# Optimization experiments

Hardware: AMD Instinct MI355X
Metric: run time of the kernel (lower is better)

## Reference

```python
import jax, jax.numpy as jnp
import numpy as np

EMBED_DIM = 64  # scale factor dim (matches head dim)


def setup_inputs() -> dict:
    key0 = jax.random.key(0)
    kq, kk, kv = jax.random.split(key0, 3)
    shape = (2, 16, 2048, 64)  # [B, H, S, D]
    return {
        "query": jax.random.normal(kq, shape, dtype=jnp.float32),
        "key": jax.random.normal(kk, shape, dtype=jnp.float32),
        "value": jax.random.normal(kv, shape, dtype=jnp.float32),
    }


def reference(query, key, value):
    # qk = Q K^T / sqrt(embed_dim); softmax over last dim; @ V
    inv_scale = jnp.sqrt(jnp.asarray(EMBED_DIM, dtype=query.dtype))
    scores = jnp.einsum("bhqd,bhkd->bhqk", query, key) / inv_scale
    probs = jax.nn.softmax(scores, axis=-1)
    # dropout_p=0.0 -> identity (eval semantics)
    return jnp.einsum("bhqk,bhkd->bhqd", probs, value)
```

## Files before the change

### kernel.cpp

```cpp
#include <hip/hip_runtime.h>
#include <hip/hip_bf16.h>

#define S_LEN 2048
#define DDIM  64
#define NT    (S_LEN / 64)
#define SCALE  0.125f
#define SCALE2 0.18033688f
#define NELEM  4194304
#define NQROW  65536
#define WC_LGKM0 0xc07f

#if __has_builtin(__builtin_amdgcn_permlane32_swap) && __has_builtin(__builtin_amdgcn_permlane16_swap)
#define HAVE_PLSWAP 1
#else
#define HAVE_PLSWAP 0
#endif

typedef __attribute__((ext_vector_type(8))) short short8;
typedef __attribute__((ext_vector_type(4))) float floatx4;

__device__ __forceinline__ short f2bf(float f) {
    union { float f; unsigned u; } v; v.f = f;
    return (short)((v.u + 0x7fffu + ((v.u >> 16) & 1u)) >> 16);
}

__device__ __forceinline__ unsigned pk2bf(float a, float b) {
#if __has_builtin(__builtin_amdgcn_cvt_pk_bf16_f32)
    auto r = __builtin_amdgcn_cvt_pk_bf16_f32(a, b);
    union { decltype(r) v; unsigned u; } c; c.v = v.v, c.v = r; return c.u;
#else
    union { float f; unsigned u; } x, y; x.f = a; y.f = b;
    unsigned lo = (x.u + 0x7fffu + ((x.u >> 16) & 1u)) >> 16;
    unsigned hi = (y.u + 0x7fffu + ((y.u >> 16) & 1u)) & 0xffff0000u;
    return lo | hi;
#endif
}

__device__ __forceinline__ float fexp2(float x) {
#if __has_builtin(__builtin_amdgcn_exp2f)
    return __builtin_amdgcn_exp2f(x);
#else
    return exp2f(x);
#endif
}

#if HAVE_PLSWAP
__device__ __forceinline__ void plswap32(unsigned &a, unsigned &b) {
    auto r = __builtin_amdgcn_permlane32_swap((int)a, (int)b, false, false);
    a = (unsigned)r[0]; b = (unsigned)r[1];
}
__device__ __forceinline__ void plswap16(unsigned &a, unsigned &b) {
    auto r = __builtin_amdgcn_permlane16_swap((int)a, (int)b, false, false);
    a = (unsigned)r[0]; b = (unsigned)r[1];
}
#endif

__global__ __launch_bounds__(256) void prep_kv(const float* __restrict__ K,
                                               const float* __restrict__ V,
                                               short* __restrict__ Kb,
                                               short* __restrict__ Vt) {
    const int bh = blockIdx.x & 31;
    const int st = blockIdx.x >> 5;
    const int t  = threadIdx.x;
    const size_t tile_off = (size_t)bh * (S_LEN * DDIM) + (size_t)st * (64 * DDIM);

    {
        const float* src = K + tile_off + t * 16;
        short* dst = Kb + tile_off + t * 16;
        #pragma unroll
        for (int h = 0; h < 2; ++h) {
            float4 a = *(const float4*)(src + h * 8);
            float4 b = *(const float4*)(src + h * 8 + 4);
            uint4 o;
            o.x = pk2bf(a.x, a.y); o.y = pk2bf(a.z, a.w);
            o.z = pk2bf(b.x, b.y); o.w = pk2bf(b.z, b.w);
            *(uint4*)(dst + h * 8) = o;
        }
    }

    {
        const int s4 = (t & 15) * 4;
        const int d4 = (t >> 4) * 4;
        const float* src = V + tile_off;
        float4 v0 = *(const float4*)(src + (size_t)(s4 + 0) * 64 + d4);
        float4 v1 = *(const float4*)(src + (size_t)(s4 + 1) * 64 + d4);
        float4 v2 = *(const float4*)(src + (size_t)(s4 + 2) * 64 + d4);
        float4 v3 = *(const float4*)(src + (size_t)(s4 + 3) * 64 + d4);
        const float* r0 = (const float*)&v0;
        const float* r1 = (const float*)&v1;
        const float* r2 = (const float*)&v2;
        const float* r3 = (const float*)&v3;
        short* dstb = Vt + (size_t)bh * (DDIM * S_LEN) + (size_t)st * 64 + s4;
        #pragma unroll
        for (int dd = 0; dd < 4; ++dd) {
            uint2 o;
            o.x = pk2bf(r0[dd], r1[dd]);
            o.y = pk2bf(r2[dd], r3[dd]);
            *(uint2*)(dstb + (size_t)(d4 + dd) * S_LEN) = o;
        }
    }
}

template <int NSPLIT>
__global__ __launch_bounds__(256) void attn_sm(
    const float* __restrict__ Q, const short* __restrict__ Kb,
    const short* __restrict__ Vt, float* __restrict__ O,
    float* __restrict__ numer, float* __restrict__ denom)
{
    __shared__ short Ks[64 * 64];
    __shared__ short Vs[64 * 64];
#if !HAVE_PLSWAP
    __shared__ short Pl[4][32 * 64];
#endif

    constexpr int NIT = NT / NSPLIT;

    const int tid  = threadIdx.x;
    const int wave = tid >> 6;
    const int lane = tid & 63;
    const int l16  = lane & 15;
    const int quad = lane >> 4;
    const int x7   = l16 & 7;

    const int bh = blockIdx.x & 31;
    const int rest = blockIdx.x >> 5;
    const int qt = rest & 15;
    const int ks = rest >> 4;
    const size_t base = (size_t)bh * (S_LEN * DDIM);

    const int ci0 = tid,        r0 = ci0 >> 3, c0 = (ci0 & 7) ^ (r0 & 7);
    const int ci1 = 256 + tid,  r1 = ci1 >> 3, c1 = (ci1 & 7) ^ (r1 & 7);
    const size_t koff = (size_t)ks * NIT * (64 * 64);
    const size_t voff = (size_t)ks * NIT * 64;
    const short* pK0 = Kb + base + koff + r0 * 64 + c0 * 8;
    const short* pK1 = Kb + base + koff + r1 * 64 + c1 * 8;
    const short* pV0 = Vt + base + voff + (size_t)r0 * S_LEN + c0 * 8;
    const short* pV1 = Vt + base + voff + (size_t)r1 * S_LEN + c1 * 8;

    short8 rk0 = *(const short8*)pK0;
    short8 rk1 = *(const short8*)pK1;
    short8 rv0 = *(const short8*)pV0;
    short8 rv1 = *(const short8*)pV1;

    short8 qf[2][2];
    #pragma unroll
    for (int nq = 0; nq < 2; ++nq) {
        const float* qp = Q + base + (size_t)(qt * 128 + wave * 32 + nq * 16 + l16) * 64 + quad * 8;
        #pragma unroll
        for (int kt = 0; kt < 2; ++kt) {
            float4 a = *(const float4*)(qp + kt * 32);
            float4 b = *(const float4*)(qp + kt * 32 + 4);
            union { unsigned u[4]; short8 s; } qc;
            qc.u[0] = pk2bf(a.x * SCALE2, a.y * SCALE2);
            qc.u[1] = pk2bf(a.z * SCALE2, a.w * SCALE2);
            qc.u[2] = pk2bf(b.x * SCALE2, b.y * SCALE2);
            qc.u[3] = pk2bf(b.z * SCALE2, b.w * SCALE2);
            qf[nq][kt] = qc.s;
        }
    }

    floatx4 oacc[2][4];
    float rs[2];
    #pragma unroll
    for (int mt = 0; mt < 2; ++mt) {
        #pragma unroll
        for (int dt = 0; dt < 4; ++dt) oacc[mt][dt] = (floatx4){0.f,0.f,0.f,0.f};
        rs[mt] = 0.f;
    }

#if !HAVE_PLSWAP
    short* Pw = &Pl[wave][0];
#endif

    for (int kb = 0; kb < NIT; ++kb) {
        if (kb) __builtin_amdgcn_s_barrier();

        *(short8*)&Ks[ci0 * 8] = rk0;
        *(short8*)&Ks[ci1 * 8] = rk1;
        *(short8*)&Vs[ci0 * 8] = rv0;
        *(short8*)&Vs[ci1 * 8] = rv1;

        if (kb + 1 < NIT) {
            const int ok = (kb + 1) * (64 * 64), ov = (kb + 1) * 64;
            rk0 = *(const short8*)(pK0 + ok);
            rk1 = *(const short8*)(pK1 + ok);
            rv0 = *(const short8*)(pV0 + ov);
            rv1 = *(const short8*)(pV1 + ov);
        }

        __builtin_amdgcn_s_waitcnt(WC_LGKM0);
        __builtin_amdgcn_s_barrier();

        floatx4 sc[2][4];
        #pragma unroll
        for (int mk = 0; mk < 4; ++mk) {
            floatx4 a0 = (floatx4){0.f,0.f,0.f,0.f};
            floatx4 a1 = (floatx4){0.f,0.f,0.f,0.f};
            #pragma unroll
            for (int kt = 0; kt < 2; ++kt) {
                const int csw = (kt * 4 + quad) ^ x7;
                short8 kf = *(const short8*)&Ks[(mk * 16 + l16) * 64 + csw * 8];
                a0 = __builtin_amdgcn_mfma_f32_16x16x32_bf16(kf, qf[0][kt], a0, 0, 0, 0);
                a1 = __builtin_amdgcn_mfma_f32_16x16x32_bf16(kf, qf[1][kt], a1, 0, 0, 0);
            }
            sc[0][mk] = a0; sc[1][mk] = a1;
        }

#if HAVE_PLSWAP
        unsigned pa[2][4], pb[2][4];
        #pragma unroll
        for (int nq = 0; nq < 2; ++nq) {
            #pragma unroll
            for (int mk = 0; mk < 4; ++mk) {
                float p0 = fexp2(sc[nq][mk][0]);
                float p1 = fexp2(sc[nq][mk][1]);
                float p2 = fexp2(sc[nq][mk][2]);
                float p3 = fexp2(sc[nq][mk][3]);
                rs[nq] += (p0 + p1) + (p2 + p3);
                pa[nq][mk] = pk2bf(p0, p1);
                pb[nq][mk] = pk2bf(p2, p3);
            }
        }

        #pragma unroll
        for (int kt = 0; kt < 2; ++kt) {
            short8 pf[2];
            #pragma unroll
            for (int nq = 0; nq < 2; ++nq) {
                unsigned a0 = pa[nq][2 * kt], a1 = pa[nq][2 * kt + 1];
                unsigned b0 = pb[nq][2 * kt], b1 = pb[nq][2 * kt + 1];
                plswap32(a0, a1); plswap16(a0, a1);
                plswap32(b0, b1); plswap16(b0, b1);
                union { unsigned u[4]; short8 s; } c;
                c.u[0] = a0; c.u[1] = b0; c.u[2] = a1; c.u[3] = b1;
                pf[nq] = c.s;
            }
            const int csw = (kt * 4 + quad) ^ x7;
            #pragma unroll
            for (int dt = 0; dt < 4; ++dt) {
                short8 vf = *(const short8*)&Vs[(dt * 16 + l16) * 64 + csw * 8];
                oacc[0][dt] = __builtin_amdgcn_mfma_f32_16x16x32_bf16(pf[0], vf, oacc[0][dt], 0, 0, 0);
                oacc[1][dt] = __builtin_amdgcn_mfma_f32_16x16x32_bf16(pf[1], vf, oacc[1][dt], 0, 0, 0);
            }
        }
#else
        #pragma unroll
        for (int nq = 0; nq < 2; ++nq) {
            const int prow = (nq * 16 + l16) * 64;
            #pragma unroll
            for (int mk = 0; mk < 4; ++mk) {
                float p0 = fexp2(sc[nq][mk][0]);
                float p1 = fexp2(sc[nq][mk][1]);
                float p2 = fexp2(sc[nq][mk][2]);
                float p3 = fexp2(sc[nq][mk][3]);
                rs[nq] += (p0 + p1) + (p2 + p3);
                uint2 pv; pv.x = pk2bf(p0, p1); pv.y = pk2bf(p2, p3);
                const int c8 = (mk * 4 + quad) ^ (2 * x7);
                *(uint2*)&Pw[prow + c8 * 4] = pv;
            }
        }
        #pragma unroll
        for (int kt = 0; kt < 2; ++kt) {
            const int csw = (kt * 4 + quad) ^ x7;
            short8 pf0 = *(const short8*)&Pw[(l16)      * 64 + csw * 8];
            short8 pf1 = *(const short8*)&Pw[(16 + l16) * 64 + csw * 8];
            #pragma unroll
            for (int dt = 0; dt < 4; ++dt) {
                short8 vf = *(const short8*)&Vs[(dt * 16 + l16) * 64 + csw * 8];
                oacc[0][dt] = __builtin_amdgcn_mfma_f32_16x16x32_bf16(pf0, vf, oacc[0][dt], 0, 0, 0);
                oacc[1][dt] = __builtin_amdgcn_mfma_f32_16x16x32_bf16(pf1, vf, oacc[1][dt], 0, 0, 0);
            }
        }
#endif
    }

    float inv[2];
    #pragma unroll
    for (int nq = 0; nq < 2; ++nq) {
        float s = rs[nq];
        s += __shfl_xor(s, 16, 64);
        s += __shfl_xor(s, 32, 64);
        if (NSPLIT == 2) {
            if (quad == 0)
                denom[(size_t)ks * NQROW + bh * S_LEN + qt * 128 + wave * 32 + nq * 16 + l16] = s;
        }
        inv[nq] = 1.0f / s;
    }

    #pragma unroll
    for (int mt = 0; mt < 2; ++mt) {
        #pragma unroll
        for (int r = 0; r < 4; ++r) {
            const int row = qt * 128 + wave * 32 + mt * 16 + quad * 4 + r;
            if (NSPLIT == 1) {
                const float d_r = __shfl(inv[mt], quad * 4 + r, 64);
                float* op = O + base + (size_t)row * 64 + l16;
                #pragma unroll
                for (int dt = 0; dt < 4; ++dt)
                    op[dt * 16] = oacc[mt][dt][r] * d_r;
            } else {
                float* np = numer + (size_t)ks * NELEM + base + (size_t)row * 64 + l16;
                #pragma unroll
                for (int dt = 0; dt < 4; ++dt)
                    np[dt * 16] = oacc[mt][dt][r];
            }
        }
    }
}

__global__ __launch_bounds__(256) void combine2(const float* __restrict__ numer,
                                                const float* __restrict__ denom,
                                                float* __restrict__ O) {
    const size_t i = ((size_t)blockIdx.x * 256 + threadIdx.x) * 4;
    const size_t q = i >> 6;
    const float inv = 1.0f / (denom[q] + denom[NQROW + q]);
    float4 n0 = *(const float4*)(numer + i);
    float4 n1 = *(const float4*)(numer + NELEM + i);
    float4 o;
    o.x = (n0.x + n1.x) * inv;
    o.y = (n0.y + n1.y) * inv;
    o.z = (n0.z + n1.z) * inv;
    o.w = (n0.w + n1.w) * inv;
    *(float4*)(O + i) = o;
}

#define BQ    64
#define BKEY  64
#define KPAD  72

__global__ __launch_bounds__(256) void attn_kernel(
    const float* __restrict__ Q, const float* __restrict__ K,
    const float* __restrict__ V, float* __restrict__ O)
{
    __shared__ short Ksh[BKEY * KPAD];
    __shared__ short Vtt[DDIM * KPAD];
    __shared__ short Pls[4][16 * KPAD];

    const int tid  = threadIdx.x;
    const int wave = tid >> 6;
    const int lane = tid & 63;
    const int l16  = lane & 15;
    const int quad = lane >> 4;

    const int bh = blockIdx.x & 31;
    const int qt = blockIdx.x >> 5;
    const size_t base = (size_t)bh * S_LEN * DDIM;

    const int qrow = qt * BQ + wave * 16 + l16;
    short8 qf[2];
    {
        const float* qp = Q + base + (size_t)qrow * DDIM + quad * 8;
        #pragma unroll
        for (int kt = 0; kt < 2; ++kt) {
            float4 a = *(const float4*)(qp + kt * 32);
            float4 b = *(const float4*)(qp + kt * 32 + 4);
            short* d = (short*)&qf[kt];
            d[0]=f2bf(a.x*SCALE); d[1]=f2bf(a.y*SCALE); d[2]=f2bf(a.z*SCALE); d[3]=f2bf(a.w*SCALE);
            d[4]=f2bf(b.x*SCALE); d[5]=f2bf(b.y*SCALE); d[6]=f2bf(b.z*SCALE); d[7]=f2bf(b.w*SCALE);
        }
    }

    float m_i[4], l_i[4];
    floatx4 oacc[4];
    #pragma unroll
    for (int r = 0; r < 4; ++r) { m_i[r] = -3.0e38f; l_i[r] = 0.f; }
    #pragma unroll
    for (int dt = 0; dt < 4; ++dt) oacc[dt] = (floatx4){0.f, 0.f, 0.f, 0.f};

    const int skey = tid >> 2;
    const int scol = (tid & 3) * 4;

    for (int kb = 0; kb < S_LEN / BKEY; ++kb) {
        const float* Kg = K + base + (size_t)kb * BKEY * DDIM + (size_t)skey * DDIM;
        const float* Vg = V + base + (size_t)kb * BKEY * DDIM + (size_t)skey * DDIM;
        #pragma unroll
        for (int i = 0; i < 4; ++i) {
            const int c = scol + i * 16;
            float4 kv = *(const float4*)(Kg + c);
            short* kd = &Ksh[skey * KPAD + c];
            kd[0]=f2bf(kv.x); kd[1]=f2bf(kv.y); kd[2]=f2bf(kv.z); kd[3]=f2bf(kv.w);
            float4 vv = *(const float4*)(Vg + c);
            Vtt[(c+0)*KPAD + skey] = f2bf(vv.x);
            Vtt[(c+1)*KPAD + skey] = f2bf(vv.y);
            Vtt[(c+2)*KPAD + skey] = f2bf(vv.z);
            Vtt[(c+3)*KPAD + skey] = f2bf(vv.w);
        }
        __syncthreads();

        floatx4 sc[4];
        #pragma unroll
        for (int nt = 0; nt < 4; ++nt) {
            floatx4 acc = (floatx4){0.f, 0.f, 0.f, 0.f};
            #pragma unroll
            for (int kt = 0; kt < 2; ++kt) {
                short8 kf = *(const short8*)&Ksh[(nt*16 + l16) * KPAD + kt*32 + quad*8];
                acc = __builtin_amdgcn_mfma_f32_16x16x32_bf16(qf[kt], kf, acc, 0, 0, 0);
            }
            sc[nt] = acc;
        }

        short* Pw = &Pls[wave][0];
        #pragma unroll
        for (int r = 0; r < 4; ++r) {
            float mx = fmaxf(fmaxf(sc[0][r], sc[1][r]), fmaxf(sc[2][r], sc[3][r]));
            #pragma unroll
            for (int off = 1; off < 16; off <<= 1)
                mx = fmaxf(mx, __shfl_xor(mx, off, 64));
            const float mnew  = fmaxf(m_i[r], mx);
            const float alpha = __expf(m_i[r] - mnew);
            m_i[r] = mnew;
            float rsum = 0.f;
            #pragma unroll
            for (int nt = 0; nt < 4; ++nt) {
                float p = __expf(sc[nt][r] - mnew);
                rsum += p;
                Pw[(quad*4 + r) * KPAD + nt*16 + l16] = f2bf(p);
            }
            #pragma unroll
            for (int off = 1; off < 16; off <<= 1)
                rsum += __shfl_xor(rsum, off, 64);
            l_i[r] = l_i[r] * alpha + rsum;
            oacc[0][r] *= alpha; oacc[1][r] *= alpha;
            oacc[2][r] *= alpha; oacc[3][r] *= alpha;
        }

        #pragma unroll
        for (int kt = 0; kt < 2; ++kt) {
            short8 pf = *(const short8*)&Pw[l16 * KPAD + kt*32 + quad*8];
            #pragma unroll
            for (int dt = 0; dt < 4; ++dt) {
                short8 vf = *(const short8*)&Vtt[(dt*16 + l16) * KPAD + kt*32 + quad*8];
                oacc[dt] = __builtin_amdgcn_mfma_f32_16x16x32_bf16(pf, vf, oacc[dt], 0, 0, 0);
            }
        }
        __syncthreads();
    }

    #pragma unroll
    for (int r = 0; r < 4; ++r) {
        const float inv = 1.0f / l_i[r];
        const int row = qt * BQ + wave * 16 + quad * 4 + r;
        float* op = O + base + (size_t)row * DDIM + l16;
        #pragma unroll
        for (int dt = 0; dt < 4; ++dt)
            op[dt * 16] = oacc[dt][r] * inv;
    }
}

extern "C" void kernel_launch(void* const* d_in, const int* in_sizes, int n_in,
                              void* d_out, int out_size, void* d_ws, size_t ws_size,
                              hipStream_t stream) {
    const float* Q = (const float*)d_in[0];
    const float* K = (const float*)d_in[1];
    const float* V = (const float*)d_in[2];
    float* O = (float*)d_out;

    const size_t prep_bytes = (size_t)NELEM * 2 * 2;
    const size_t split_bytes = prep_bytes + (size_t)2 * NELEM * 4
                             + (size_t)2 * NQROW * 4;

    if (ws_size >= split_bytes) {
        short* Kb  = (short*)d_ws;
        short* Vtp = (short*)d_ws + NELEM;
        float* num = (float*)((char*)d_ws + prep_bytes);
        float* den = num + (size_t)2 * NELEM;
        prep_kv<<<dim3(1024), dim3(256), 0, stream>>>(K, V, Kb, Vtp);
        attn_sm<2><<<dim3(1024), dim3(256), 0, stream>>>(Q, Kb, Vtp, nullptr, num, den);
        combine2<<<dim3(NELEM / 1024), dim3(256), 0, stream>>>(num, den, O);
    } else if (ws_size >= prep_bytes) {
        short* Kb  = (short*)d_ws;
        short* Vtp = (short*)d_ws + NELEM;
        prep_kv<<<dim3(1024), dim3(256), 0, stream>>>(K, V, Kb, Vtp);
        attn_sm<1><<<dim3(512), dim3(256), 0, stream>>>(Q, Kb, Vtp, O, nullptr, nullptr);
    } else {
        attn_kernel<<<dim3(1024), dim3(256), 0, stream>>>(Q, K, V, O);
    }
}
```

Baseline: 150.7 us.

## Fuse split-K combine into attention kernel via last-arriver atomic counter

```diff
diff --git a/kernel.cpp b/kernel.cpp
--- a/kernel.cpp
+++ b/kernel.cpp
@@ -25,15 +25,10 @@
 }
 
 __device__ __forceinline__ unsigned pk2bf(float a, float b) {
-#if __has_builtin(__builtin_amdgcn_cvt_pk_bf16_f32)
-    auto r = __builtin_amdgcn_cvt_pk_bf16_f32(a, b);
-    union { decltype(r) v; unsigned u; } c; c.v = v.v, c.v = r; return c.u;
-#else
     union { float f; unsigned u; } x, y; x.f = a; y.f = b;
     unsigned lo = (x.u + 0x7fffu + ((x.u >> 16) & 1u)) >> 16;
     unsigned hi = (y.u + 0x7fffu + ((y.u >> 16) & 1u)) & 0xffff0000u;
     return lo | hi;
-#endif
 }
 
 __device__ __forceinline__ float fexp2(float x) {
@@ -58,11 +53,17 @@
 __global__ __launch_bounds__(256) void prep_kv(const float* __restrict__ K,
                                                const float* __restrict__ V,
                                                short* __restrict__ Kb,
-                                               short* __restrict__ Vt) {
+                                               short* __restrict__ Vt,
+                                               unsigned* __restrict__ cnt) {
     const int bh = blockIdx.x & 31;
     const int st = blockIdx.x >> 5;
     const int t  = threadIdx.x;
     const size_t tile_off = (size_t)bh * (S_LEN * DDIM) + (size_t)st * (64 * DDIM);
+
+    if (cnt && blockIdx.x == 0) {
+        cnt[t] = 0u;
+        cnt[t + 256] = 0u;
+    }
 
     {
         const float* src = K + tile_off + t * 16;
@@ -105,10 +106,12 @@
 __global__ __launch_bounds__(256) void attn_sm(
     const float* __restrict__ Q, const short* __restrict__ Kb,
     const short* __restrict__ Vt, float* __restrict__ O,
-    float* __restrict__ numer, float* __restrict__ denom)
+    float* __restrict__ numer, float* __restrict__ denom,
+    unsigned* __restrict__ cnt)
 {
     __shared__ short Ks[64 * 64];
     __shared__ short Vs[64 * 64];
+    __shared__ unsigned sflag;
 #if !HAVE_PLSWAP
     __shared__ short Pl[4][32 * 64];
 #endif
@@ -274,35 +277,74 @@
 #endif
     }
 
-    float inv[2];
+    float sred[2];
     #pragma unroll
     for (int nq = 0; nq < 2; ++nq) {
         float s = rs[nq];
         s += __shfl_xor(s, 16, 64);
         s += __shfl_xor(s, 32, 64);
-        if (NSPLIT == 2) {
-            if (quad == 0)
-                denom[(size_t)ks * NQROW + bh * S_LEN + qt * 128 + wave * 32 + nq * 16 + l16] = s;
-        }
-        inv[nq] = 1.0f / s;
-    }
-
-    #pragma unroll
-    for (int mt = 0; mt < 2; ++mt) {
-        #pragma unroll
-        for (int r = 0; r < 4; ++r) {
-            const int row = qt * 128 + wave * 32 + mt * 16 + quad * 4 + r;
-            if (NSPLIT == 1) {
-                const float d_r = __shfl(inv[mt], quad * 4 + r, 64);
+        sred[nq] = s;
+    }
+
+    if (NSPLIT == 1) {
+        #pragma unroll
+        for (int mt = 0; mt < 2; ++mt) {
+            const float invm = 1.0f / sred[mt];
+            #pragma unroll
+            for (int r = 0; r < 4; ++r) {
+                const int row = qt * 128 + wave * 32 + mt * 16 + quad * 4 + r;
+                const float d_r = __shfl(invm, quad * 4 + r, 64);
                 float* op = O + base + (size_t)row * 64 + l16;
                 #pragma unroll
                 for (int dt = 0; dt < 4; ++dt)
                     op[dt * 16] = oacc[mt][dt][r] * d_r;
-            } else {
+            }
+        }
+    } else {
+        if (quad == 0) {
+            #pragma unroll
+            for (int nq = 0; nq < 2; ++nq)
+                denom[(size_t)ks * NQROW + bh * S_LEN + qt * 128 + wave * 32 + nq * 16 + l16] = sred[nq];
+        }
+        #pragma unroll
+        for (int mt = 0; mt < 2; ++mt) {
+            #pragma unroll
+            for (int r = 0; r < 4; ++r) {
+                const int row = qt * 128 + wave * 32 + mt * 16 + quad * 4 + r;
                 float* np = numer + (size_t)ks * NELEM + base + (size_t)row * 64 + l16;
                 #pragma unroll
                 for (int dt = 0; dt < 4; ++dt)
                     np[dt * 16] = oacc[mt][dt][r];
+            }
+        }
+
+        __threadfence();
+        __syncthreads();
+        if (tid == 0) sflag = atomicAdd(&cnt[(bh << 4) + qt], 1u);
+        __syncthreads();
+        if (sflag == 0) return;
+        __threadfence();
+
+        const int kso = 1 - ks;
+        const float* onum = numer + (size_t)kso * NELEM + base;
+        const float* oden = denom + (size_t)kso * NQROW + bh * S_LEN + qt * 128 + wave * 32;
+
+        float invt[2];
+        #pragma unroll
+        for (int nq = 0; nq < 2; ++nq)
+            invt[nq] = 1.0f / (sred[nq] + oden[nq * 16 + l16]);
+
+        #pragma unroll
+        for (int mt = 0; mt < 2; ++mt) {
+            #pragma unroll
+            for (int r = 0; r < 4; ++r) {
+                const int row = qt * 128 + wave * 32 + mt * 16 + quad * 4 + r;
+                const float it = __shfl(invt[mt], quad * 4 + r, 64);
+                const float* np = onum + (size_t)row * 64 + l16;
+                float* op = O + base + (size_t)row * 64 + l16;
+                #pragma unroll
+                for (int dt = 0; dt < 4; ++dt)
+                    op[dt * 16] = (oacc[mt][dt][r] + np[dt * 16]) * it;
             }
         }
     }
@@ -458,20 +500,29 @@
     const size_t prep_bytes = (size_t)NELEM * 2 * 2;
     const size_t split_bytes = prep_bytes + (size_t)2 * NELEM * 4
                              + (size_t)2 * NQROW * 4;
-
-    if (ws_size >= split_bytes) {
+    const size_t fused_bytes = split_bytes + 2048;
+
+    if (ws_size >= fused_bytes) {
         short* Kb  = (short*)d_ws;
         short* Vtp = (short*)d_ws + NELEM;
         float* num = (float*)((char*)d_ws + prep_bytes);
         float* den = num + (size_t)2 * NELEM;
-        prep_kv<<<dim3(1024), dim3(256), 0, stream>>>(K, V, Kb, Vtp);
-        attn_sm<2><<<dim3(1024), dim3(256), 0, stream>>>(Q, Kb, Vtp, nullptr, num, den);
+        unsigned* cnt = (unsigned*)((char*)d_ws + split_bytes);
+        prep_kv<<<dim3(1024), dim3(256), 0, stream>>>(K, V, Kb, Vtp, cnt);
+        attn_sm<2><<<dim3(1024), dim3(256), 0, stream>>>(Q, Kb, Vtp, O, num, den, cnt);
+    } else if (ws_size >= split_bytes) {
+        short* Kb  = (short*)d_ws;
+        short* Vtp = (short*)d_ws + NELEM;
+        float* num = (float*)((char*)d_ws + prep_bytes);
+        float* den = num + (size_t)2 * NELEM;
+        prep_kv<<<dim3(1024), dim3(256), 0, stream>>>(K, V, Kb, Vtp, nullptr);
+        attn_sm<2><<<dim3(1024), dim3(256), 0, stream>>>(Q, Kb, Vtp, nullptr, num, den, nullptr);
         combine2<<<dim3(NELEM / 1024), dim3(256), 0, stream>>>(num, den, O);
     } else if (ws_size >= prep_bytes) {
         short* Kb  = (short*)d_ws;
         short* Vtp = (short*)d_ws + NELEM;
-        prep_kv<<<dim3(1024), dim3(256), 0, stream>>>(K, V, Kb, Vtp);
-        attn_sm<1><<<dim3(512), dim3(256), 0, stream>>>(Q, Kb, Vtp, O, nullptr, nullptr);
+        prep_kv<<<dim3(1024), dim3(256), 0, stream>>>(K, V, Kb, Vtp, nullptr);
+        attn_sm<1><<<dim3(512), dim3(256), 0, stream>>>(Q, Kb, Vtp, O, nullptr, nullptr, nullptr);
     } else {
         attn_kernel<<<dim3(1024), dim3(256), 0, stream>>>(Q, K, V, O);
     }
```

After: 307.2 us. 104% more time.

## Fuse split-K attention halves into one 512-thread block with LDS combine

Applied to the files above, without the earlier changes.

```diff
diff --git a/kernel.cpp b/kernel.cpp
--- a/kernel.cpp
+++ b/kernel.cpp
@@ -25,15 +25,10 @@
 }
 
 __device__ __forceinline__ unsigned pk2bf(float a, float b) {
-#if __has_builtin(__builtin_amdgcn_cvt_pk_bf16_f32)
-    auto r = __builtin_amdgcn_cvt_pk_bf16_f32(a, b);
-    union { decltype(r) v; unsigned u; } c; c.v = v.v, c.v = r; return c.u;
-#else
     union { float f; unsigned u; } x, y; x.f = a; y.f = b;
     unsigned lo = (x.u + 0x7fffu + ((x.u >> 16) & 1u)) >> 16;
     unsigned hi = (y.u + 0x7fffu + ((y.u >> 16) & 1u)) & 0xffff0000u;
     return lo | hi;
-#endif
 }
 
 __device__ __forceinline__ float fexp2(float x) {
@@ -101,35 +96,36 @@
     }
 }
 
-template <int NSPLIT>
-__global__ __launch_bounds__(256) void attn_sm(
+__global__ __launch_bounds__(512) void attn_sm8(
     const float* __restrict__ Q, const short* __restrict__ Kb,
-    const short* __restrict__ Vt, float* __restrict__ O,
-    float* __restrict__ numer, float* __restrict__ denom)
+    const short* __restrict__ Vt, float* __restrict__ O)
 {
-    __shared__ short Ks[64 * 64];
-    __shared__ short Vs[64 * 64];
+    __shared__ short Ks[2][64 * 64];
+    __shared__ short Vs[2][64 * 64];
+    __shared__ float Dl[128];
 #if !HAVE_PLSWAP
-    __shared__ short Pl[4][32 * 64];
-#endif
-
-    constexpr int NIT = NT / NSPLIT;
+    __shared__ short Pl[8][32 * 64];
+#endif
+
+    constexpr int NIT = NT / 2;
 
     const int tid  = threadIdx.x;
     const int wave = tid >> 6;
+    const int grp  = wave >> 2;
+    const int w4   = wave & 3;
     const int lane = tid & 63;
     const int l16  = lane & 15;
     const int quad = lane >> 4;
     const int x7   = l16 & 7;
 
     const int bh = blockIdx.x & 31;
-    const int rest = blockIdx.x >> 5;
-    const int qt = rest & 15;
-    const int ks = rest >> 4;
+    const int qt = blockIdx.x >> 5;
+    const int ks = grp;
     const size_t base = (size_t)bh * (S_LEN * DDIM);
 
-    const int ci0 = tid,        r0 = ci0 >> 3, c0 = (ci0 & 7) ^ (r0 & 7);
-    const int ci1 = 256 + tid,  r1 = ci1 >> 3, c1 = (ci1 & 7) ^ (r1 & 7);
+    const int g   = tid & 255;
+    const int ci0 = g,        r0 = ci0 >> 3, c0 = (ci0 & 7) ^ (r0 & 7);
+    const int ci1 = 256 + g,  r1 = ci1 >> 3, c1 = (ci1 & 7) ^ (r1 & 7);
     const size_t koff = (size_t)ks * NIT * (64 * 64);
     const size_t voff = (size_t)ks * NIT * 64;
     const short* pK0 = Kb + base + koff + r0 * 64 + c0 * 8;
@@ -145,7 +141,7 @@
     short8 qf[2][2];
     #pragma unroll
     for (int nq = 0; nq < 2; ++nq) {
-        const float* qp = Q + base + (size_t)(qt * 128 + wave * 32 + nq * 16 + l16) * 64 + quad * 8;
+        const float* qp = Q + base + (size_t)(qt * 128 + w4 * 32 + nq * 16 + l16) * 64 + quad * 8;
         #pragma unroll
         for (int kt = 0; kt < 2; ++kt) {
             float4 a = *(const float4*)(qp + kt * 32);
@@ -168,6 +164,8 @@
         rs[mt] = 0.f;
     }
 
+    short* Ksg = &Ks[grp][0];
+    short* Vsg = &Vs[grp][0];
 #if !HAVE_PLSWAP
     short* Pw = &Pl[wave][0];
 #endif
@@ -175,10 +173,10 @@
     for (int kb = 0; kb < NIT; ++kb) {
         if (kb) __builtin_amdgcn_s_barrier();
 
-        *(short8*)&Ks[ci0 * 8] = rk0;
-        *(short8*)&Ks[ci1 * 8] = rk1;
-        *(short8*)&Vs[ci0 * 8] = rv0;
-        *(short8*)&Vs[ci1 * 8] = rv1;
+        *(short8*)&Ksg[ci0 * 8] = rk0;
+        *(short8*)&Ksg[ci1 * 8] = rk1;
+        *(short8*)&Vsg[ci0 * 8] = rv0;
+        *(short8*)&Vsg[ci1 * 8] = rv1;
 
         if (kb + 1 < NIT) {
             const int ok = (kb + 1) * (64 * 64), ov = (kb + 1) * 64;
@@ -199,7 +197,7 @@
             #pragma unroll
             for (int kt = 0; kt < 2; ++kt) {
                 const int csw = (kt * 4 + quad) ^ x7;
-                short8 kf = *(const short8*)&Ks[(mk * 16 + l16) * 64 + csw * 8];
+                short8 kf = *(const short8*)&Ksg[(mk * 16 + l16) * 64 + csw * 8];
                 a0 = __builtin_amdgcn_mfma_f32_16x16x32_bf16(kf, qf[0][kt], a0, 0, 0, 0);
                 a1 = __builtin_amdgcn_mfma_f32_16x16x32_bf16(kf, qf[1][kt], a1, 0, 0, 0);
             }
@@ -238,7 +236,7 @@
             const int csw = (kt * 4 + quad) ^ x7;
             #pragma unroll
             for (int dt = 0; dt < 4; ++dt) {
-                short8 vf = *(const short8*)&Vs[(dt * 16 + l16) * 64 + csw * 8];
+                short8 vf = *(const short8*)&Vsg[(dt * 16 + l16) * 64 + csw * 8];
                 oacc[0][dt] = __builtin_amdgcn_mfma_f32_16x16x32_bf16(pf[0], vf, oacc[0][dt], 0, 0, 0);
                 oacc[1][dt] = __builtin_amdgcn_mfma_f32_16x16x32_bf16(pf[1], vf, oacc[1][dt], 0, 0, 0);
             }
@@ -266,7 +264,7 @@
             short8 pf1 = *(const short8*)&Pw[(16 + l16) * 64 + csw * 8];
             #pragma unroll
             for (int dt = 0; dt < 4; ++dt) {
-                short8 vf = *(const short8*)&Vs[(dt * 16 + l16) * 64 + csw * 8];
+                short8 vf = *(const short8*)&Vsg[(dt * 16 + l16) * 64 + csw * 8];
                 oacc[0][dt] = __builtin_amdgcn_mfma_f32_16x16x32_bf16(pf0, vf, oacc[0][dt], 0, 0, 0);
                 oacc[1][dt] = __builtin_amdgcn_mfma_f32_16x16x32_bf16(pf1, vf, oacc[1][dt], 0, 0, 0);
             }
@@ -274,54 +272,51 @@
 #endif
     }
 
-    float inv[2];
+    float sred[2];
     #pragma unroll
     for (int nq = 0; nq < 2; ++nq) {
         float s = rs[nq];
         s += __shfl_xor(s, 16, 64);
         s += __shfl_xor(s, 32, 64);
-        if (NSPLIT == 2) {
-            if (quad == 0)
-                denom[(size_t)ks * NQROW + bh * S_LEN + qt * 128 + wave * 32 + nq * 16 + l16] = s;
-        }
-        inv[nq] = 1.0f / s;
-    }
-
+        sred[nq] = s;
+    }
+
+    if (grp == 1 && quad == 0) {
+        Dl[w4 * 32 + l16]      = sred[0];
+        Dl[w4 * 32 + 16 + l16] = sred[1];
+    }
+    __syncthreads();
+
+    float invt[2];
+    if (grp == 0) {
+        invt[0] = 1.0f / (sred[0] + Dl[w4 * 32 + l16]);
+        invt[1] = 1.0f / (sred[1] + Dl[w4 * 32 + 16 + l16]);
+    }
+
+    float* Nb = (float*)&Ks[0][0];
     #pragma unroll
     for (int mt = 0; mt < 2; ++mt) {
-        #pragma unroll
-        for (int r = 0; r < 4; ++r) {
-            const int row = qt * 128 + wave * 32 + mt * 16 + quad * 4 + r;
-            if (NSPLIT == 1) {
-                const float d_r = __shfl(inv[mt], quad * 4 + r, 64);
+        if (grp == 1) {
+            #pragma unroll
+            for (int dt = 0; dt < 4; ++dt)
+                #pragma unroll
+                for (int r = 0; r < 4; ++r)
+                    Nb[(dt * 4 + r) * 256 + w4 * 64 + lane] = oacc[mt][dt][r];
+        }
+        __syncthreads();
+        if (grp == 0) {
+            #pragma unroll
+            for (int r = 0; r < 4; ++r) {
+                const int row = qt * 128 + w4 * 32 + mt * 16 + quad * 4 + r;
+                const float it = __shfl(invt[mt], quad * 4 + r, 64);
                 float* op = O + base + (size_t)row * 64 + l16;
                 #pragma unroll
                 for (int dt = 0; dt < 4; ++dt)
-                    op[dt * 16] = oacc[mt][dt][r] * d_r;
-            } else {
-                float* np = numer + (size_t)ks * NELEM + base + (size_t)row * 64 + l16;
-                #pragma unroll
-                for (int dt = 0; dt < 4; ++dt)
-                    np[dt * 16] = oacc[mt][dt][r];
-            }
-        }
-    }
-}
-
-__global__ __launch_bounds__(256) void combine2(const float* __restrict__ numer,
-                                                const float* __restrict__ denom,
-                                                float* __restrict__ O) {
-    const size_t i = ((size_t)blockIdx.x * 256 + threadIdx.x) * 4;
-    const size_t q = i >> 6;
-    const float inv = 1.0f / (denom[q] + denom[NQROW + q]);
-    float4 n0 = *(const float4*)(numer + i);
-    float4 n1 = *(const float4*)(numer + NELEM + i);
-    float4 o;
-    o.x = (n0.x + n1.x) * inv;
-    o.y = (n0.y + n1.y) * inv;
-    o.z = (n0.z + n1.z) * inv;
-    o.w = (n0.w + n1.w) * inv;
-    *(float4*)(O + i) = o;
+                    op[dt * 16] = (oacc[mt][dt][r] + Nb[(dt * 4 + r) * 256 + w4 * 64 + lane]) * it;
+            }
+        }
+        __syncthreads();
+    }
 }
 
 #define BQ    64
@@ -456,22 +451,12 @@
     float* O = (float*)d_out;
 
     const size_t prep_bytes = (size_t)NELEM * 2 * 2;
-    const size_t split_bytes = prep_bytes + (size_t)2 * NELEM * 4
-                             + (size_t)2 * NQROW * 4;
-
-    if (ws_size >= split_bytes) {
-        short* Kb  = (short*)d_ws;
-        short* Vtp = (short*)d_ws + NELEM;
-        float* num = (float*)((char*)d_ws + prep_bytes);
-        float* den = num + (size_t)2 * NELEM;
-        prep_kv<<<dim3(1024), dim3(256), 0, stream>>>(K, V, Kb, Vtp);
-        attn_sm<2><<<dim3(1024), dim3(256), 0, stream>>>(Q, Kb, Vtp, nullptr, num, den);
-        combine2<<<dim3(NELEM / 1024), dim3(256), 0, stream>>>(num, den, O);
-    } else if (ws_size >= prep_bytes) {
+
+    if (ws_size >= prep_bytes) {
         short* Kb  = (short*)d_ws;
         short* Vtp = (short*)d_ws + NELEM;
         prep_kv<<<dim3(1024), dim3(256), 0, stream>>>(K, V, Kb, Vtp);
-        attn_sm<1><<<dim3(512), dim3(256), 0, stream>>>(Q, Kb, Vtp, O, nullptr, nullptr);
+        attn_sm8<<<dim3(512), dim3(512), 0, stream>>>(Q, Kb, Vtp, O);
     } else {
         attn_kernel<<<dim3(1024), dim3(256), 0, stream>>>(Q, K, V, O);
     }
```

Result: faster. 144.2 us (-4.3%).
